# Kernel tuning notes

Measured on AMD Instinct MI355X. Metric: run time of the kernel, lower is better.

The kernel has to match this reference:

```python
import jax, jax.numpy as jnp
import numpy as np
from jax import lax

B = 16384
BN_EPS = 1e-5


def setup_inputs() -> dict:
    key = jax.random.key(0)
    ks = jax.random.split(key, 6)
    x = jax.random.normal(ks[0], (B, 1, 28, 28), jnp.float32)
    conv_w = jax.random.normal(ks[1], (4, 1, 3, 3), jnp.float32) * 0.2
    bn_gamma = jnp.ones((4,), jnp.float32)
    bn_beta = jnp.zeros((4,), jnp.float32)
    bn_mean = jnp.zeros((4,), jnp.float32)
    bn_var = jnp.ones((4,), jnp.float32)
    var_params = jax.random.normal(ks[2], (4,), jnp.float32)
    lin_w = jax.random.normal(ks[3], (10, 784), jnp.float32) * 0.03
    lin_b = jnp.zeros((10,), jnp.float32)
    return {"x": x, "conv_w": conv_w, "bn_gamma": bn_gamma, "bn_beta": bn_beta,
            "bn_mean": bn_mean, "bn_var": bn_var, "var_params": var_params,
            "lin_w": lin_w, "lin_b": lin_b}


def _ry_w0(s, theta):
    # apply RY(theta) to wire 0 (axis -2) of real state s[..., 2, 2]
    c, si = jnp.cos(theta * 0.5), jnp.sin(theta * 0.5)
    R = jnp.stack([jnp.stack([c, -si]), jnp.stack([si, c])])
    return jnp.einsum('ij,...jk->...ik', R, s)


def _ry_w1(s, theta):
    # apply RY(theta) to wire 1 (axis -1)
    c, si = jnp.cos(theta * 0.5), jnp.sin(theta * 0.5)
    R = jnp.stack([jnp.stack([c, -si]), jnp.stack([si, c])])
    return jnp.einsum('ij,...kj->...ki', R, s)


def _quantum_features(img, v):
    # img: [B, 28, 28] -> features [B, 196*4] (patch-major, 4 expvals each)
    b = img.shape[0]
    p = img.reshape(b, 14, 2, 14, 2).transpose(0, 1, 3, 2, 4)  # [B,14,14,2,2]
    # encoding RYs on same wire compose: angles a = p0+p2 (wire0), b = p1+p3 (wire1)
    ha = (p[..., 0, 0] + p[..., 1, 0]) * 0.5
    hb = (p[..., 0, 1] + p[..., 1, 1]) * 0.5
    w0 = jnp.stack([jnp.cos(ha), jnp.sin(ha)], axis=-1)
    w1 = jnp.stack([jnp.cos(hb), jnp.sin(hb)], axis=-1)
    s = w0[..., :, None] * w1[..., None, :]  # real statevector [B,14,14,2,2]
    # CNOT(control=0, target=1): flip wire1 where wire0 == 1
    s = jnp.stack([s[..., 0, :], s[..., 1, ::-1]], axis=-2)
    s = _ry_w0(s, v[0])
    s = _ry_w1(s, v[1])
    # CNOT(control=1, target=0): flip wire0 where wire1 == 1
    s = jnp.stack([s[..., :, 0], s[..., ::-1, 1]], axis=-1)
    s = _ry_w0(s, v[2])
    s = _ry_w1(s, v[3])
    z0 = jnp.sum(s[..., 0, :] ** 2 - s[..., 1, :] ** 2, axis=-1)
    z1 = jnp.sum(s[..., :, 0] ** 2 - s[..., :, 1] ** 2, axis=-1)
    x0 = 2.0 * jnp.sum(s[..., 0, :] * s[..., 1, :], axis=-1)
    x1 = 2.0 * jnp.sum(s[..., :, 0] * s[..., :, 1], axis=-1)
    return jnp.stack([z0, z1, x0, x1], axis=-1).reshape(b, -1)  # [B,784]


def reference(x, conv_w, bn_gamma, bn_beta, bn_mean, bn_var, var_params, lin_w, lin_b):
    b = x.shape[0]
    # classical branch: conv(s=2,p=1) -> BN (eval) -> ReLU -> flatten
    h = lax.conv_general_dilated(x, conv_w, window_strides=(2, 2),
                                 padding=((1, 1), (1, 1)))  # [B,4,14,14]
    inv = bn_gamma / jnp.sqrt(bn_var + BN_EPS)
    h = h * inv[None, :, None, None] + (bn_beta - bn_mean * inv)[None, :, None, None]
    h = jnp.maximum(h, 0.0)
    cls_out = h.reshape(b, -1)  # [B,784]
    # quantum branch over 2x2 patches
    q_out = _quantum_features(x[:, 0], var_params)  # [B,784]
    fused = cls_out + q_out
    logits = fused @ lin_w.T + lin_b
    return jax.nn.log_softmax(logits, axis=-1)
```

## Files before the change

kernel.cpp:

```cpp
#include <hip/hip_runtime.h>
#include <math.h>


typedef __fp16 h2 __attribute__((ext_vector_type(2)));
typedef __fp16 h4 __attribute__((ext_vector_type(4)));
typedef __fp16 h8 __attribute__((ext_vector_type(8)));
typedef float  f2 __attribute__((ext_vector_type(2)));
typedef float  f32x4 __attribute__((ext_vector_type(4)));

#define NSAMP 8
#define FSTRIDE 808

__device__ __forceinline__ float rfl(float v) {
    return __int_as_float(__builtin_amdgcn_readfirstlane(__float_as_int(v)));
}

__device__ __forceinline__ f2 max0(f2 v) {
    f2 r; r.x = fmaxf(v.x, 0.f); r.y = fmaxf(v.y, 0.f); return r;
}

__device__ __forceinline__ void load_patch(const float* __restrict__ xs, int p,
                                           float a[9]) {
    unsigned ii = (unsigned)p / 14u;
    int j  = p - (int)ii * 14;
    int rm = (int)ii * 56 + 2 * j;
    float2 Rm = *(const float2*)(xs + rm);
    float2 Rb = *(const float2*)(xs + rm + 28);
    int rt = rm - 28;  rt  = (rt  > 0) ? rt  : 0;
    float2 Rt = *(const float2*)(xs + rt);
    int olt = rm - 30; olt = (olt > 0) ? olt : 0;
    float2 Lt = *(const float2*)(xs + olt);
    int olm = rm - 2;  olm = (olm > 0) ? olm : 0;
    float2 Lm = *(const float2*)(xs + olm);
    float2 Lb = *(const float2*)(xs + olm + 28);
    float mt = (ii > 0u) ? 1.f : 0.f;
    float ml = (j  > 0 ) ? 1.f : 0.f;
    a[0] = Lt.y * (mt * ml); a[1] = Rt.x * mt; a[2] = Rt.y * mt;
    a[3] = Lm.y * ml;        a[4] = Rm.x;      a[5] = Rm.y;
    a[6] = Lb.y * ml;        a[7] = Rb.x;      a[8] = Rb.y;
}

__global__ __launch_bounds__(256, 6)
void quanv_fused(const float* __restrict__ x,
                 const float* __restrict__ conv_w,
                 const float* __restrict__ bn_gamma,
                 const float* __restrict__ bn_beta,
                 const float* __restrict__ bn_mean,
                 const float* __restrict__ bn_var,
                 const float* __restrict__ var_params,
                 const float* __restrict__ lin_w,
                 const float* __restrict__ lin_b,
                 float* __restrict__ out, int B)
{
    __shared__ __align__(16) __fp16 clsB[NSAMP * FSTRIDE];
    __shared__ __align__(16) __fp16 qB[NSAMP * FSTRIDE];

    const int tid  = threadIdx.x;
    const int lane = tid & 63;
    const int wave = tid >> 6;

    if (tid < 128) {
        int r = tid >> 4, buf = (tid >> 3) & 1, w = tid & 7;
        int* wp = (int*)((buf ? qB : clsB) + r * FSTRIDE + 784);
        wp[w] = 0;
    }

    float inv[4], addc[4];
    #pragma unroll
    for (int c = 0; c < 4; ++c) {
        float iv = bn_gamma[c] * rsqrtf(bn_var[c] + 1e-5f);
        inv[c]  = rfl(iv);
        addc[c] = rfl(bn_beta[c] - bn_mean[c] * iv);
    }
    float cv[4], sv[4];
    #pragma unroll
    for (int k = 0; k < 4; ++k) {
        float s, c;
        __sincosf(var_params[k] * 0.5f, &s, &c);
        sv[k] = rfl(s); cv[k] = rfl(c);
    }

    const int s_loc = tid >> 5;
    const int q32   = tid & 31;
    const int sg    = blockIdx.x * NSAMP + s_loc;
    const int sgc   = (sg < B) ? sg : (B - 1);
    const float* xs = x + (size_t)sgc * 784;
    __fp16* clsRow  = clsB + s_loc * FSTRIDE;
    __fp16* qRow    = qB   + s_loc * FSTRIDE;

    #pragma unroll
    for (int h = 0; h < 4; ++h) {
        const int pa = q32 + 64 * h, pb = pa + 32;
        const int pac = (pa < 196) ? pa : 195;
        const int pbc = (pb < 196) ? pb : 195;

        float A[9], Bv[9];
        load_patch(xs, pac, A);
        load_patch(xs, pbc, Bv);
        f2 aP[9];
        #pragma unroll
        for (int k2 = 0; k2 < 9; ++k2) { f2 t = {A[k2], Bv[k2]}; aP[k2] = t; }

        f2 hc[4];
        #pragma unroll
        for (int c = 0; c < 4; ++c) {
            f2 hx = aP[0] * conv_w[c*9+0];
            hx += aP[1] * conv_w[c*9+1];
            hx += aP[2] * conv_w[c*9+2];
            hx += aP[3] * conv_w[c*9+3];
            hx += aP[4] * conv_w[c*9+4];
            hx += aP[5] * conv_w[c*9+5];
            hx += aP[6] * conv_w[c*9+6];
            hx += aP[7] * conv_w[c*9+7];
            hx += aP[8] * conv_w[c*9+8];
            hc[c] = max0(hx * inv[c] + addc[c]);
        }
        if (pa < 196) {
            h2 ca = __builtin_amdgcn_cvt_pkrtz(hc[0].x, hc[1].x);
            h2 cb = __builtin_amdgcn_cvt_pkrtz(hc[2].x, hc[3].x);
            __fp16* cr = clsRow + pac;
            cr[0] = ca.x; cr[196] = ca.y; cr[392] = cb.x; cr[588] = cb.y;
        }
        if (pb < 196) {
            h2 ca = __builtin_amdgcn_cvt_pkrtz(hc[0].y, hc[1].y);
            h2 cb = __builtin_amdgcn_cvt_pkrtz(hc[2].y, hc[3].y);
            __fp16* cr = clsRow + pbc;
            cr[0] = ca.x; cr[196] = ca.y; cr[392] = cb.x; cr[588] = cb.y;
        }

        f2 haP = 0.5f * (aP[4] + aP[7]);
        f2 hbP = 0.5f * (aP[5] + aP[8]);
        float s0x, c0x, s0y, c0y, s1x, c1x, s1y, c1y;
        __sincosf(haP.x, &s0x, &c0x); __sincosf(haP.y, &s0y, &c0y);
        __sincosf(hbP.x, &s1x, &c1x); __sincosf(hbP.y, &s1y, &c1y);
        f2 c0 = {c0x, c0y}, s0 = {s0x, s0y};
        f2 c1 = {c1x, c1y}, s1 = {s1x, s1y};
        f2 m00 = c0*c1, m01 = c0*s1;
        f2 m10 = s0*s1, m11 = s0*c1;
        f2 t00 = cv[0]*m00 - sv[0]*m10, t01 = cv[0]*m01 - sv[0]*m11;
        f2 t10 = sv[0]*m00 + cv[0]*m10, t11 = sv[0]*m01 + cv[0]*m11;
        f2 u00 = cv[1]*t00 - sv[1]*t01, u01 = sv[1]*t00 + cv[1]*t01;
        f2 u10 = cv[1]*t10 - sv[1]*t11, u11 = sv[1]*t10 + cv[1]*t11;
        f2 w01 = u11, w11 = u01;
        f2 p00 = cv[2]*u00 - sv[2]*u10, p01 = cv[2]*w01 - sv[2]*w11;
        f2 p10 = sv[2]*u00 + cv[2]*u10, p11 = sv[2]*w01 + cv[2]*w11;
        f2 q00 = cv[3]*p00 - sv[3]*p01, q01 = sv[3]*p00 + cv[3]*p01;
        f2 q10 = cv[3]*p10 - sv[3]*p11, q11 = sv[3]*p10 + cv[3]*p11;

        f2 z0 = q00*q00 + q01*q01 - q10*q10 - q11*q11;
        f2 z1 = q00*q00 + q10*q10 - q01*q01 - q11*q11;
        f2 x0 = 2.f * (q00*q10 + q01*q11);
        f2 x1 = 2.f * (q00*q01 + q10*q11);
        if (pa < 196) {
            h2 zz = __builtin_amdgcn_cvt_pkrtz(z0.x, z1.x);
            h2 xx = __builtin_amdgcn_cvt_pkrtz(x0.x, x1.x);
            h4 qv = {zz.x, zz.y, xx.x, xx.y};
            *(h4*)(qRow + 4 * pac) = qv;
        }
        if (pb < 196) {
            h2 zz = __builtin_amdgcn_cvt_pkrtz(z0.y, z1.y);
            h2 xx = __builtin_amdgcn_cvt_pkrtz(x0.y, x1.y);
            h4 qv = {zz.x, zz.y, xx.x, xx.y};
            *(h4*)(qRow + 4 * pbc) = qv;
        }
    }

    const int bcol = lane & 15, bkg = lane >> 4;
    const __fp16 hz = (__fp16)0.f;
    const h8 hz8 = {hz, hz, hz, hz, hz, hz, hz, hz};
    h8 bfrag[7];
    #pragma unroll
    for (int t = 0; t < 7; ++t) {
        int st = wave * 7 + t;
        int kb = st * 32 + bkg * 8;
        h8 bf = hz8;
        if (bcol < 10 && kb < 784) {
            const float4* lw4 = (const float4*)(lin_w + bcol * 784 + kb);
            float4 v0 = lw4[0], v1 = lw4[1];
            h2 p0 = __builtin_amdgcn_cvt_pkrtz(v0.x, v0.y);
            h2 p1 = __builtin_amdgcn_cvt_pkrtz(v0.z, v0.w);
            h2 p2 = __builtin_amdgcn_cvt_pkrtz(v1.x, v1.y);
            h2 p3 = __builtin_amdgcn_cvt_pkrtz(v1.z, v1.w);
            h8 tv = {p0.x, p0.y, p1.x, p1.y, p2.x, p2.y, p3.x, p3.y};
            bf = tv;
        }
        bfrag[t] = bf;
    }

    __syncthreads();

    f32x4 acc = {0.f, 0.f, 0.f, 0.f};
    {
        const int arow = lane & 15, akg = lane >> 4;
        #pragma unroll
        for (int t = 0; t < 7; ++t) {
            int st = wave * 7 + t;
            if (st < 25) {
                h8 a = hz8;
                if (arow < NSAMP) {
                    int off = arow * FSTRIDE + st * 32 + akg * 8;
                    a = *(const h8*)(clsB + off) + *(const h8*)(qB + off);
                }
                acc = __builtin_amdgcn_mfma_f32_16x16x32_f16(a, bfrag[t], acc, 0, 0, 0);
            }
        }
    }

    __syncthreads();
    float* pw = (float*)clsB;
    if (lane < 32) {
        const int col = lane & 15, rb = (lane >> 4) * 4;
        #pragma unroll
        for (int r = 0; r < 4; ++r)
            pw[(wave * 8 + rb + r) * 16 + col] = acc[r];
    }
    __syncthreads();

    if (tid < 128) {
        const int c  = tid & 15;
        const int sl = tid >> 4;
        float L = pw[sl * 16 + c] + pw[(8 + sl) * 16 + c]
                + pw[(16 + sl) * 16 + c] + pw[(24 + sl) * 16 + c];
        L = (c < 10) ? (L + lin_b[c]) : -1e30f;
        float mx = L;
        mx = fmaxf(mx, __shfl_xor(mx, 1, 16));
        mx = fmaxf(mx, __shfl_xor(mx, 2, 16));
        mx = fmaxf(mx, __shfl_xor(mx, 4, 16));
        mx = fmaxf(mx, __shfl_xor(mx, 8, 16));
        float se = (c < 10) ? __expf(L - mx) : 0.f;
        se += __shfl_xor(se, 1, 16);
        se += __shfl_xor(se, 2, 16);
        se += __shfl_xor(se, 4, 16);
        se += __shfl_xor(se, 8, 16);
        const int sg2 = blockIdx.x * NSAMP + sl;
        if (c < 10 && sg2 < B)
            out[(size_t)sg2 * 10 + c] = L - mx - __logf(se);
    }
}

extern "C" void kernel_launch(void* const* d_in, const int* in_sizes, int n_in,
                              void* d_out, int out_size, void* d_ws, size_t ws_size,
                              hipStream_t stream) {
    const float* x          = (const float*)d_in[0];
    const float* conv_w     = (const float*)d_in[1];
    const float* bn_gamma   = (const float*)d_in[2];
    const float* bn_beta    = (const float*)d_in[3];
    const float* bn_mean    = (const float*)d_in[4];
    const float* bn_var     = (const float*)d_in[5];
    const float* var_params = (const float*)d_in[6];
    const float* lin_w      = (const float*)d_in[7];
    const float* lin_b      = (const float*)d_in[8];
    float* out = (float*)d_out;

    const int B = in_sizes[0] / 784;
    const int blocks = (B + NSAMP - 1) / NSAMP;
    quanv_fused<<<blocks, 256, 0, stream>>>(x, conv_w, bn_gamma, bn_beta, bn_mean,
                                            bn_var, var_params, lin_w, lin_b, out, B);
}
```

Before: 108.2 us.

## Process ten samples per block with flat patch-to-thread mapping

Raises samples per block from 8 to 10 so the 16-row MFMA tile carries more real rows. Patch work is remapped flatly, with each thread taking patches pp and pp+98 of a sample, so fewer lanes sit idle than with the old 32-thread-per-sample scheme, which padded 196 patches up to 256 slots. The partial-logit staging is widened to 16 rows per wave. It uses more shared memory per block and lowers the occupancy hint from 6 to 5 blocks per CU.

```diff
diff --git a/kernel.cpp b/kernel.cpp
--- a/kernel.cpp
+++ b/kernel.cpp
@@ -8,7 +8,7 @@
 typedef float  f2 __attribute__((ext_vector_type(2)));
 typedef float  f32x4 __attribute__((ext_vector_type(4)));
 
-#define NSAMP 8
+#define NSAMP 10
 #define FSTRIDE 808
 
 __device__ __forceinline__ float rfl(float v) {
@@ -40,7 +40,7 @@
     a[6] = Lb.y * ml;        a[7] = Rb.x;      a[8] = Rb.y;
 }
 
-__global__ __launch_bounds__(256, 6)
+__global__ __launch_bounds__(256, 5)
 void quanv_fused(const float* __restrict__ x,
                  const float* __restrict__ conv_w,
                  const float* __restrict__ bn_gamma,
@@ -59,7 +59,7 @@
     const int lane = tid & 63;
     const int wave = tid >> 6;
 
-    if (tid < 128) {
+    if (tid < NSAMP * 16) {
         int r = tid >> 4, buf = (tid >> 3) & 1, w = tid & 7;
         int* wp = (int*)((buf ? qB : clsB) + r * FSTRIDE + 784);
         wp[w] = 0;
@@ -80,23 +80,23 @@
         sv[k] = rfl(s); cv[k] = rfl(c);
     }
 
-    const int s_loc = tid >> 5;
-    const int q32   = tid & 31;
-    const int sg    = blockIdx.x * NSAMP + s_loc;
-    const int sgc   = (sg < B) ? sg : (B - 1);
-    const float* xs = x + (size_t)sgc * 784;
-    __fp16* clsRow  = clsB + s_loc * FSTRIDE;
-    __fp16* qRow    = qB   + s_loc * FSTRIDE;
+    const int sbase = blockIdx.x * NSAMP;
 
     #pragma unroll
     for (int h = 0; h < 4; ++h) {
-        const int pa = q32 + 64 * h, pb = pa + 32;
-        const int pac = (pa < 196) ? pa : 195;
-        const int pbc = (pb < 196) ? pb : 195;
+        const int g  = tid + 256 * h;
+        const bool act = (g < NSAMP * 98);
+        const int gc = act ? g : (NSAMP * 98 - 1);
+        const int s_loc = (int)((unsigned)gc / 98u);
+        const int pp    = gc - 98 * s_loc;
+
+        const int sg  = sbase + s_loc;
+        const int sgc = (sg < B) ? sg : (B - 1);
+        const float* xs = x + (size_t)sgc * 784;
 
         float A[9], Bv[9];
-        load_patch(xs, pac, A);
-        load_patch(xs, pbc, Bv);
+        load_patch(xs, pp, A);
+        load_patch(xs, pp + 98, Bv);
         f2 aP[9];
         #pragma unroll
         for (int k2 = 0; k2 < 9; ++k2) { f2 t = {A[k2], Bv[k2]}; aP[k2] = t; }
@@ -114,18 +114,6 @@
             hx += aP[7] * conv_w[c*9+7];
             hx += aP[8] * conv_w[c*9+8];
             hc[c] = max0(hx * inv[c] + addc[c]);
-        }
-        if (pa < 196) {
-            h2 ca = __builtin_amdgcn_cvt_pkrtz(hc[0].x, hc[1].x);
-            h2 cb = __builtin_amdgcn_cvt_pkrtz(hc[2].x, hc[3].x);
-            __fp16* cr = clsRow + pac;
-            cr[0] = ca.x; cr[196] = ca.y; cr[392] = cb.x; cr[588] = cb.y;
-        }
-        if (pb < 196) {
-            h2 ca = __builtin_amdgcn_cvt_pkrtz(hc[0].y, hc[1].y);
-            h2 cb = __builtin_amdgcn_cvt_pkrtz(hc[2].y, hc[3].y);
-            __fp16* cr = clsRow + pbc;
-            cr[0] = ca.x; cr[196] = ca.y; cr[392] = cb.x; cr[588] = cb.y;
         }
 
         f2 haP = 0.5f * (aP[4] + aP[7]);
@@ -151,17 +139,30 @@
         f2 z1 = q00*q00 + q10*q10 - q01*q01 - q11*q11;
         f2 x0 = 2.f * (q00*q10 + q01*q11);
         f2 x1 = 2.f * (q00*q01 + q10*q11);
-        if (pa < 196) {
-            h2 zz = __builtin_amdgcn_cvt_pkrtz(z0.x, z1.x);
-            h2 xx = __builtin_amdgcn_cvt_pkrtz(x0.x, x1.x);
-            h4 qv = {zz.x, zz.y, xx.x, xx.y};
-            *(h4*)(qRow + 4 * pac) = qv;
-        }
-        if (pb < 196) {
-            h2 zz = __builtin_amdgcn_cvt_pkrtz(z0.y, z1.y);
-            h2 xx = __builtin_amdgcn_cvt_pkrtz(x0.y, x1.y);
-            h4 qv = {zz.x, zz.y, xx.x, xx.y};
-            *(h4*)(qRow + 4 * pbc) = qv;
+
+        if (act) {
+            __fp16* clsRow = clsB + s_loc * FSTRIDE;
+            __fp16* qRow   = qB   + s_loc * FSTRIDE;
+            {
+                h2 ca = __builtin_amdgcn_cvt_pkrtz(hc[0].x, hc[1].x);
+                h2 cb = __builtin_amdgcn_cvt_pkrtz(hc[2].x, hc[3].x);
+                __fp16* cr = clsRow + pp;
+                cr[0] = ca.x; cr[196] = ca.y; cr[392] = cb.x; cr[588] = cb.y;
+                h2 zz = __builtin_amdgcn_cvt_pkrtz(z0.x, z1.x);
+                h2 xx = __builtin_amdgcn_cvt_pkrtz(x0.x, x1.x);
+                h4 qv = {zz.x, zz.y, xx.x, xx.y};
+                *(h4*)(qRow + 4 * pp) = qv;
+            }
+            {
+                h2 ca = __builtin_amdgcn_cvt_pkrtz(hc[0].y, hc[1].y);
+                h2 cb = __builtin_amdgcn_cvt_pkrtz(hc[2].y, hc[3].y);
+                __fp16* cr = clsRow + pp + 98;
+                cr[0] = ca.x; cr[196] = ca.y; cr[392] = cb.x; cr[588] = cb.y;
+                h2 zz = __builtin_amdgcn_cvt_pkrtz(z0.y, z1.y);
+                h2 xx = __builtin_amdgcn_cvt_pkrtz(x0.y, x1.y);
+                h4 qv = {zz.x, zz.y, xx.x, xx.y};
+                *(h4*)(qRow + 4 * (pp + 98)) = qv;
+            }
         }
     }
 
@@ -208,19 +209,19 @@
 
     __syncthreads();
     float* pw = (float*)clsB;
-    if (lane < 32) {
+    {
         const int col = lane & 15, rb = (lane >> 4) * 4;
         #pragma unroll
         for (int r = 0; r < 4; ++r)
-            pw[(wave * 8 + rb + r) * 16 + col] = acc[r];
+            pw[(wave * 16 + rb + r) * 16 + col] = acc[r];
     }
     __syncthreads();
 
-    if (tid < 128) {
+    if (tid < NSAMP * 16) {
         const int c  = tid & 15;
         const int sl = tid >> 4;
-        float L = pw[sl * 16 + c] + pw[(8 + sl) * 16 + c]
-                + pw[(16 + sl) * 16 + c] + pw[(24 + sl) * 16 + c];
+        float L = pw[sl * 16 + c] + pw[(16 + sl) * 16 + c]
+                + pw[(32 + sl) * 16 + c] + pw[(48 + sl) * 16 + c];
         L = (c < 10) ? (L + lin_b[c]) : -1e30f;
         float mx = L;
         mx = fmaxf(mx, __shfl_xor(mx, 1, 16));
```

New measurement: 108.9 us. About the same (+0.6%).
